# Kernel optimization log

Measured on AMD Instinct MI355X. Metric: run time of the kernel, lower is better.

## Reference

```python
import jax, jax.numpy as jnp
import numpy as np

B, L, SIZE, HEADS, AH, NBR, KER, DEPTH = 64, 512, 128, 8, 16, 15, 16, 3
MAXD = 20.0
N = B * L
EDGE = KER + 3 + 9 + 1  # 29


def _normalize(v):
    return v / (jnp.linalg.norm(v, axis=-1, keepdims=True) + 1e-8)


def _frames(pos):
    # local orientation frame per residue from consecutive CA displacements
    u = _normalize(pos[1:] - pos[:-1])            # (N-1,3)
    up = jnp.concatenate([u[:1], u], axis=0)      # u_{i-1}
    un = jnp.concatenate([u, u[-1:]], axis=0)     # u_i
    b = _normalize(up - un)
    n = _normalize(jnp.cross(up, un))
    return jnp.stack([b, n, jnp.cross(b, n)], axis=-1)  # (N,3,3)


def setup_inputs() -> dict:
    key = jax.random.key(0)
    ks = jax.random.split(key, 16)
    g = lambda i, shape, s=1.0: jax.random.normal(ks[i], shape, jnp.float32) * s
    return {
        "tertiary": g(0, (N, 3, 3), 10.0),
        "sequence": g(1, (N, 20)),
        "subgraph_indices": jnp.arange(N, dtype=jnp.int32) // L,
        "knn_noise": g(2, (B, L, L)),
        "embed_w": g(3, (27, SIZE), 0.1), "embed_b": jnp.zeros((SIZE,), jnp.float32),
        "wq": g(4, (DEPTH, SIZE, HEADS * AH), 0.08),
        "wk": g(5, (DEPTH, SIZE + EDGE, HEADS * AH), 0.08),
        "wv": g(6, (DEPTH, SIZE + EDGE, HEADS * AH), 0.08),
        "wo": g(7, (DEPTH, HEADS * AH, SIZE), 0.08),
        "mlp_w1": g(8, (DEPTH, SIZE, SIZE), 0.08), "mlp_b1": jnp.zeros((DEPTH, SIZE), jnp.float32),
        "mlp_w2": g(9, (DEPTH, SIZE, SIZE), 0.08), "mlp_b2": jnp.zeros((DEPTH, SIZE), jnp.float32),
        "mlp_w3": g(10, (DEPTH, SIZE, SIZE), 0.08), "mlp_b3": jnp.zeros((DEPTH, SIZE), jnp.float32),
        "pool_w": g(11, (4, SIZE, SIZE, 3), 0.05), "pool_b": jnp.zeros((4, SIZE), jnp.float32),
        "energy_w": g(12, (SIZE, 1), 0.1), "energy_b": jnp.zeros((1,), jnp.float32),
    }


def _forward(tertiary, sequence, knn_noise, embed_w, embed_b, wq, wk, wv, wo,
             mlp_w1, mlp_b1, mlp_w2, mlp_b2, mlp_w3, mlp_b3,
             pool_w, pool_b, energy_w, energy_b):
    pos = tertiary[:, 1]                                   # (N,3) CA positions
    R = _frames(pos)                                       # (N,3,3)
    # ---- kNN per contiguous protein group with noisy distances ----
    pg = pos.reshape(B, L, 3)
    dist = jnp.linalg.norm(pg[:, :, None] - pg[:, None, :], axis=-1)  # (B,L,L)
    closeness = -dist + 3.0 * knn_noise
    idx = jax.lax.top_k(closeness, NBR)[1]                 # (B,L,NBR) local
    nbr = (idx + (jnp.arange(B) * L)[:, None, None]).reshape(N, NBR)
    # ---- RBF relative encoding (RelativeStructure.message) ----
    dvec = pos[nbr] - pos[:, None]                         # (N,NBR,3)
    d = jnp.linalg.norm(dvec, axis=-1)                     # (N,NBR)
    mu = jnp.linspace(0.0, MAXD, KER)
    sigma = MAXD / KER
    rbf = jnp.exp(-(((d[..., None] - mu) / sigma) ** 2))   # (N,NBR,KER)
    dirs = jnp.einsum('nrc,nkr->nkc', R, dvec / (d[..., None] + 1e-8))
    relrot = jnp.einsum('nrc,nkrd->nkcd', R, R[nbr]).reshape(N, NBR, 9)
    ind = jnp.arange(N, dtype=tertiary.dtype)
    relind = (ind[nbr] - ind[:, None])[..., None]
    edge = jnp.concatenate([rbf, dirs, relrot, relind], axis=-1)  # (N,NBR,EDGE)
    # ---- structured graph-attention encoder ----
    h = jnp.ones((N, 27), tertiary.dtype) @ embed_w + embed_b
    inv_sqrt = 1.0 / np.sqrt(AH).astype(np.float32)
    for l in range(DEPTH):
        q = (h @ wq[l]).reshape(N, HEADS, AH)
        kv = jnp.concatenate([h[nbr], edge], axis=-1)      # (N,NBR,SIZE+EDGE)
        k = (kv @ wk[l]).reshape(N, NBR, HEADS, AH)
        v = (kv @ wv[l]).reshape(N, NBR, HEADS, AH)
        logits = jnp.einsum('nhd,nkhd->nhk', q, k) * inv_sqrt
        a = jax.nn.softmax(logits, axis=-1)
        o = jnp.einsum('nhk,nkhd->nhd', a, v).reshape(N, HEADS * AH) @ wo[l]
        h = h + o
        m = jax.nn.relu(h @ mlp_w1[l] + mlp_b1[l])
        m = jax.nn.relu(m @ mlp_w2[l] + mlp_b2[l])
        h = h + m @ mlp_w3[l] + mlp_b3[l]
    # ---- scatter-pad pool: residual conv + maxpool(2), x4, then length-sum ----
    x = h.reshape(B, L, SIZE).transpose(0, 2, 1)           # (B,SIZE,L)
    for i in range(4):
        y = jax.lax.conv_general_dilated(
            x, pool_w[i], (1,), ((1, 1),),
            dimension_numbers=('NCH', 'OIH', 'NCH')) + pool_b[i][None, :, None]
        x = x + jax.nn.leaky_relu(y, 0.01)
        Lc = x.shape[-1]
        x = x.reshape(B, SIZE, Lc // 2, 2).max(axis=-1)
    pooled = x.sum(axis=-1)                                # (B,SIZE)
    return pooled @ energy_w + energy_b                    # (B,1)


def reference(tertiary, sequence, subgraph_indices, knn_noise, embed_w, embed_b,
              wq, wk, wv, wo, mlp_w1, mlp_b1, mlp_w2, mlp_b2, mlp_w3, mlp_b3,
              pool_w, pool_b, energy_w, energy_b):
    # subgraph_indices encodes contiguous equal-size groups (arange // L)
    return _forward(tertiary, sequence, knn_noise, embed_w, embed_b, wq, wk, wv, wo,
                    mlp_w1, mlp_b1, mlp_w2, mlp_b2, mlp_w3, mlp_b3,
                    pool_w, pool_b, energy_w, energy_b)
```

## Files before the change

### kernel.cpp

```cpp
#include <hip/hip_runtime.h>
#include <math.h>

#define N_TOT 32768
#define NNBR 15
#define APW 8
#define ELP 36
#define ETP 20
#define PLP 20

#define KNB 4096
#define FRB 128
#define PRB 3392

typedef __attribute__((ext_vector_type(8))) _Float16 f16x8;
typedef __attribute__((ext_vector_type(2))) _Float16 f16x2;
typedef __attribute__((ext_vector_type(4))) float f32x4;

#define CBAR() __asm__ volatile("" ::: "memory")

__device__ __forceinline__ _Float16 f2h(float x) { return (_Float16)x; }

template <int CTRL>
__device__ __forceinline__ unsigned long long dpp_max_u64(unsigned long long x) {
  unsigned lo = (unsigned)__builtin_amdgcn_update_dpp(
      0, (int)(unsigned)x, CTRL, 0xf, 0xf, true);
  unsigned hi = (unsigned)__builtin_amdgcn_update_dpp(
      0, (int)(unsigned)(x >> 32), CTRL, 0xf, 0xf, true);
  unsigned long long y = ((unsigned long long)hi << 32) | lo;
  return y > x ? y : x;
}

__device__ __forceinline__ void ins3(unsigned long long k,
                                     unsigned long long& m1,
                                     unsigned long long& m2,
                                     unsigned long long& m3) {
  unsigned long long t1 = k > m1 ? k : m1;
  unsigned long long r1 = k > m1 ? m1 : k;
  unsigned long long t2 = r1 > m2 ? r1 : m2;
  unsigned long long r2 = r1 > m2 ? m2 : r1;
  unsigned long long t3 = r2 > m3 ? r2 : m3;
  m1 = t1; m2 = t2; m3 = t3;
}

__global__ __launch_bounds__(256) void k_pre(
    const float* __restrict__ tert, const float* __restrict__ noise,
    int* __restrict__ nbr, float* __restrict__ pos, float* __restrict__ R,
    const float* __restrict__ wq, const float* __restrict__ wk,
    const float* __restrict__ wv, const float* __restrict__ wo,
    const float* __restrict__ w1, const float* __restrict__ w2,
    const float* __restrict__ w3, _Float16* __restrict__ wbt,
    _Float16* __restrict__ wqk, _Float16* __restrict__ wpe,
    const float* __restrict__ pw, _Float16* __restrict__ wct,
    const float* __restrict__ ew, const float* __restrict__ ebias,
    _Float16* __restrict__ h) {
  __shared__ float posL[512 * 3];
  __shared__ float hvS[128];
  int bb = blockIdx.x, tid = threadIdx.x;
  if (bb < KNB) {
    int b = bb >> 6;
    int n0 = b << 9;
    for (int i = tid; i < 1536; i += 256) {
      int r = i / 3, c = i - r * 3;
      posL[i] = tert[(size_t)(n0 + r) * 9 + 3 + c];
    }
    __syncthreads();
    int wave = tid >> 6, lane = tid & 63;
    int l = lane & 31;
    int rloc = (bb & 63) * 8 + wave * 2 + (lane >> 5);
    int row = n0 + rloc;
    const float* nrow = noise + (size_t)row * 512;
    float pix = posL[rloc * 3 + 0];
    float piy = posL[rloc * 3 + 1];
    float piz = posL[rloc * 3 + 2];
    unsigned long long m1 = 0ull, m2 = 0ull, m3 = 0ull;
#pragma unroll
    for (int jj = 0; jj < 16; jj++) {
      int j = l + jj * 32;
      float dx = posL[j * 3 + 0] - pix;
      float dy = posL[j * 3 + 1] - piy;
      float dz = posL[j * 3 + 2] - piz;
      float c = -sqrtf(dx * dx + dy * dy + dz * dz) + 3.f * nrow[j];
      unsigned u = __float_as_uint(c);
      unsigned s = u ^ (unsigned)(((int)u >> 31) | (int)0x80000000);
      unsigned long long k = ((unsigned long long)s << 9) | (unsigned)(511 - j);
      ins3(k, m1, m2, m3);
    }
    int jmine = 0;
#pragma unroll 1
    for (int it = 0; it < NNBR; it++) {
      unsigned long long r = m1;
      r = dpp_max_u64<0x111>(r);
      r = dpp_max_u64<0x112>(r);
      r = dpp_max_u64<0x114>(r);
      r = dpp_max_u64<0x118>(r);
      r = dpp_max_u64<0x142>(r);
      unsigned gloA = (unsigned)__builtin_amdgcn_readlane((int)(unsigned)r, 31);
      unsigned ghiA = (unsigned)__builtin_amdgcn_readlane((int)(unsigned)(r >> 32), 31);
      unsigned gloB = (unsigned)__builtin_amdgcn_readlane((int)(unsigned)r, 63);
      unsigned ghiB = (unsigned)__builtin_amdgcn_readlane((int)(unsigned)(r >> 32), 63);
      int jA = 511 - (int)(gloA & 511u);
      int jB = 511 - (int)(gloB & 511u);
      int j = (lane & 32) ? jB : jA;
      if (l == it) jmine = j;
      bool win = ((j & 31) == l);
      if (win) { m1 = m2; m2 = m3; m3 = 0ull; }
      if (__any((int)(win && m1 == 0ull))) {
        if (win && m1 == 0ull) {
          unsigned long long gthr = (lane & 32)
              ? (((unsigned long long)ghiB << 32) | gloB)
              : (((unsigned long long)ghiA << 32) | gloA);
          unsigned long long a1 = 0ull, a2 = 0ull, a3 = 0ull;
#pragma unroll 1
          for (int jj = 0; jj < 16; jj++) {
            int j2 = l + jj * 32;
            float dx = posL[j2 * 3 + 0] - pix;
            float dy = posL[j2 * 3 + 1] - piy;
            float dz = posL[j2 * 3 + 2] - piz;
            float c = -sqrtf(dx * dx + dy * dy + dz * dz) + 3.f * nrow[j2];
            unsigned u = __float_as_uint(c);
            unsigned s = u ^ (unsigned)(((int)u >> 31) | (int)0x80000000);
            unsigned long long k = ((unsigned long long)s << 9) | (unsigned)(511 - j2);
            if (k < gthr) ins3(k, a1, a2, a3);
          }
          m1 = a1; m2 = a2; m3 = a3;
        }
      }
    }
    if (l < NNBR) nbr[(size_t)row * NNBR + l] = n0 + jmine;
  } else if (bb < KNB + FRB) {
    int n = (bb - KNB) * 256 + tid;
    if (n >= N_TOT) return;
    float px = tert[n * 9 + 3], py = tert[n * 9 + 4], pz = tert[n * 9 + 5];
    pos[n * 3 + 0] = px; pos[n * 3 + 1] = py; pos[n * 3 + 2] = pz;
    int i0 = (n > 0) ? (n - 1) : 0;
    int i1 = (n < N_TOT - 1) ? n : (N_TOT - 2);
    float ax = tert[(i0 + 1) * 9 + 3] - tert[i0 * 9 + 3];
    float ay = tert[(i0 + 1) * 9 + 4] - tert[i0 * 9 + 4];
    float az = tert[(i0 + 1) * 9 + 5] - tert[i0 * 9 + 5];
    float il = 1.f / (sqrtf(ax * ax + ay * ay + az * az) + 1e-8f);
    float ux = ax * il, uy = ay * il, uz = az * il;
    float cx = tert[(i1 + 1) * 9 + 3] - tert[i1 * 9 + 3];
    float cy = tert[(i1 + 1) * 9 + 4] - tert[i1 * 9 + 4];
    float cz = tert[(i1 + 1) * 9 + 5] - tert[i1 * 9 + 5];
    il = 1.f / (sqrtf(cx * cx + cy * cy + cz * cz) + 1e-8f);
    float vx = cx * il, vy = cy * il, vz = cz * il;
    float bx = ux - vx, by = uy - vy, bz = uz - vz;
    il = 1.f / (sqrtf(bx * bx + by * by + bz * bz) + 1e-8f);
    bx *= il; by *= il; bz *= il;
    float nx = uy * vz - uz * vy;
    float ny = uz * vx - ux * vz;
    float nz = ux * vy - uy * vx;
    il = 1.f / (sqrtf(nx * nx + ny * ny + nz * nz) + 1e-8f);
    nx *= il; ny *= il; nz *= il;
    float ex = by * nz - bz * ny;
    float ey = bz * nx - bx * nz;
    float ez = bx * ny - by * nx;
    float* Rn = R + (size_t)n * 9;
    Rn[0] = bx; Rn[1] = nx; Rn[2] = ex;
    Rn[3] = by; Rn[4] = ny; Rn[5] = ey;
    Rn[6] = bz; Rn[7] = nz; Rn[8] = ez;
  } else {
    int pb2 = bb - (KNB + FRB);
    if (pb2 < 1344) {
      int idx = pb2 * 256 + tid;
      int lL = idx / (7 * 16384);
      int r = idx % (7 * 16384);
      int w = r / 16384;
      int e = r % 16384;
      int k = e >> 7, n = e & 127;
      float val;
      switch (w) {
        case 0: val = wq[(size_t)lL * 16384 + e]; break;
        case 1: val = wk[(size_t)lL * 157 * 128 + e]; break;
        case 2: val = wv[(size_t)lL * 157 * 128 + e]; break;
        case 3: val = wo[(size_t)lL * 16384 + e]; break;
        case 4: val = w1[(size_t)lL * 16384 + e]; break;
        case 5: val = w2[(size_t)lL * 16384 + e]; break;
        default: val = w3[(size_t)lL * 16384 + e]; break;
      }
      wbt[(size_t)(lL * 7 + w) * 16384 + n * 128 + k] = f2h(val);
    } else if (pb2 < 1728) {
      int idx = (pb2 - 1344) * 256 + tid;
      int lL = idx / 32768;
      int r = idx % 32768;
      int blk = r >> 14;
      int jp = (r >> 7) & 127;
      int c = r & 127;
      int j = blk * 128 + jp;
      int hh = j >> 5, e = j & 31;
      float val = 0.f;
      if (e < 29) {
        const float* wqp = wq + (size_t)lL * 16384 + (size_t)c * 128 + hh * 16;
        const float* wkp = wk + (size_t)lL * 157 * 128 + (size_t)(128 + e) * 128 + hh * 16;
        float s = 0.f;
#pragma unroll
        for (int d = 0; d < 16; d++) s = fmaf(wqp[d], wkp[d], s);
        val = 0.25f * s;
      }
      wqk[(size_t)idx] = f2h(val);
    } else if (pb2 < 2112) {
      int idx = (pb2 - 1728) * 256 + tid;
      int lL = idx / 32768;
      int r = idx % 32768;
      int blk = r >> 14;
      int cout = (r >> 7) & 127;
      int jp = r & 127;
      int j = blk * 128 + jp;
      float val = 0.f;
      if (j < 232) {
        int e = j >> 3, hh = j & 7;
        const float* wvp = wv + (size_t)lL * 157 * 128 + (size_t)(128 + e) * 128 + hh * 16;
        const float* wop = wo + (size_t)lL * 16384 + (size_t)(hh * 16) * 128 + cout;
#pragma unroll
        for (int d = 0; d < 16; d++) val = fmaf(wvp[d], wop[d * 128], val);
      }
      wpe[(size_t)idx] = f2h(val);
    } else if (pb2 < 2880) {
      int idx = (pb2 - 2112) * 256 + tid;
      int kt = idx % 3;
      int rest = idx / 3;
      int i = rest % 128; rest /= 128;
      int oo = rest % 128;
      int s = rest / 128;
      wct[(((size_t)s * 3 + kt) * 128 + oo) * 128 + i] = f2h(pw[idx]);
    } else {
      int vb = pb2 - 2880;
      if (tid < 128) {
        float s = ebias[tid];
#pragma unroll
        for (int i = 0; i < 27; i++) s += ew[i * 128 + tid];
        hvS[tid] = s;
      }
      __syncthreads();
      size_t total = (size_t)N_TOT * 128;
      for (size_t j = (size_t)vb * 256 + tid; j < total; j += (size_t)512 * 256)
        h[j] = f2h(hvS[j & 127]);
    }
  }
}

__global__ __launch_bounds__(256) void k_edge(const float* __restrict__ pos,
                                              const float* __restrict__ R,
                                              const int* __restrict__ nbr,
                                              _Float16* __restrict__ edge) {
  int idx = blockIdx.x * 256 + threadIdx.x;
  if (idx >= N_TOT * NNBR) return;
  int n = idx / NNBR;
  int m = nbr[idx];
  float dx = pos[m * 3 + 0] - pos[n * 3 + 0];
  float dy = pos[m * 3 + 1] - pos[n * 3 + 1];
  float dz = pos[m * 3 + 2] - pos[n * 3 + 2];
  float d = sqrtf(dx * dx + dy * dy + dz * dz);
  _Float16 eb[32];
#pragma unroll
  for (int j = 0; j < 16; j++) {
    float mu = (20.f / 15.f) * (float)j;
    float t = (d - mu) * 0.8f;
    eb[j] = f2h(__expf(-t * t));
  }
  float inv = 1.f / (d + 1e-8f);
  float ux = dx * inv, uy = dy * inv, uz = dz * inv;
  float Rn[9], Rm[9];
#pragma unroll
  for (int j = 0; j < 9; j++) { Rn[j] = R[(size_t)n * 9 + j]; Rm[j] = R[(size_t)m * 9 + j]; }
#pragma unroll
  for (int cc = 0; cc < 3; cc++)
    eb[16 + cc] = f2h(Rn[0 * 3 + cc] * ux + Rn[1 * 3 + cc] * uy + Rn[2 * 3 + cc] * uz);
#pragma unroll
  for (int cc = 0; cc < 3; cc++)
#pragma unroll
    for (int dd = 0; dd < 3; dd++)
      eb[19 + cc * 3 + dd] = f2h(Rn[0 * 3 + cc] * Rm[0 * 3 + dd] +
                                 Rn[1 * 3 + cc] * Rm[1 * 3 + dd] +
                                 Rn[2 * 3 + cc] * Rm[2 * 3 + dd]);
  eb[28] = f2h((float)(m - n));
  eb[29] = (_Float16)0.f; eb[30] = (_Float16)0.f; eb[31] = (_Float16)0.f;
  _Float16* e = edge + (size_t)idx * 32;
#pragma unroll
  for (int v = 0; v < 4; v++)
    *(uint4*)(e + v * 8) = *(const uint4*)(&eb[v * 8]);
}

__device__ __forceinline__ void stage_w(const _Float16* __restrict__ W, _Float16* Ws, int tid) {
  for (int j = tid; j < 2048; j += 256) {
    int row = j >> 4, seg = (j & 15) * 8;
    *(uint4*)&Ws[row * 136 + seg] = *(const uint4*)(W + (size_t)row * 128 + seg);
  }
}
__device__ __forceinline__ void stage_x(const _Float16* __restrict__ src, _Float16* X,
                                        int tid, int rowstride) {
  for (int j = tid; j < 1024; j += 256) {
    int row = j >> 4, seg = (j & 15) * 8;
    *(uint4*)&X[row * 136 + seg] = *(const uint4*)(src + (size_t)row * rowstride + seg);
  }
}
template <bool RESET>
__device__ __forceinline__ void gemm_tile_t(const _Float16* X, const _Float16* Ws,
                                            int wrow, int l16, int quad, f32x4 acc[8]) {
  if (RESET) {
#pragma unroll
    for (int t = 0; t < 8; t++) acc[t] = (f32x4){0.f, 0.f, 0.f, 0.f};
  }
#pragma unroll
  for (int kk = 0; kk < 4; kk++) {
    f16x8 a = *(const f16x8*)&X[(wrow + l16) * 136 + kk * 32 + quad * 8];
#pragma unroll
    for (int t = 0; t < 8; t++) {
      f16x8 b = *(const f16x8*)&Ws[(t * 16 + l16) * 136 + kk * 32 + quad * 8];
      acc[t] = __builtin_amdgcn_mfma_f32_16x16x32_f16(a, b, acc[t], 0, 0, 0);
    }
  }
}

__global__ __launch_bounds__(256) void k_qkv(const _Float16* __restrict__ A,
                                             const _Float16* __restrict__ Wqt,
                                             const _Float16* __restrict__ Wkt,
                                             const _Float16* __restrict__ Wvt,
                                             const _Float16* __restrict__ Wqk0,
                                             const _Float16* __restrict__ Wqk1,
                                             _Float16* __restrict__ q, _Float16* __restrict__ hk,
                                             _Float16* __restrict__ hv, _Float16* __restrict__ qkw) {
  __shared__ _Float16 X[64 * 136];
  __shared__ _Float16 Ws[128 * 136];
  int tid = threadIdx.x, r0 = blockIdx.x * 64;
  int lane = tid & 63, quad = lane >> 4, l16 = lane & 15, wrow = (tid >> 6) * 16;
  stage_x(A + (size_t)r0 * 128, X, tid, 128);
  const _Float16* wts[5] = {Wqt, Wkt, Wvt, Wqk0, Wqk1};
  f32x4 acc[8];
  for (int w = 0; w < 5; w++) {
    __syncthreads();
    stage_w(wts[w], Ws, tid);
    __syncthreads();
    gemm_tile_t<true>(X, Ws, wrow, l16, quad, acc);
#pragma unroll
    for (int t = 0; t < 8; t++) {
      int col = t * 16 + l16;
#pragma unroll
      for (int r = 0; r < 4; r++) {
        float v = acc[t][r];
        int rowg = r0 + wrow + quad * 4 + r;
        if (w < 3) {
          _Float16* C = (w == 0) ? q : (w == 1) ? hk : hv;
          C[(size_t)rowg * 128 + col] = f2h(v);
        } else {
          qkw[(size_t)rowg * 256 + (w - 3) * 128 + col] = f2h(v);
        }
      }
    }
  }
}

__global__ __launch_bounds__(256) void k_post(const _Float16* __restrict__ o,
                                              const _Float16* __restrict__ pe_g,
                                              _Float16* __restrict__ h,
                                              const _Float16* __restrict__ Wot,
                                              const _Float16* __restrict__ Wpe0,
                                              const _Float16* __restrict__ Wpe1,
                                              const _Float16* __restrict__ W1t, const float* __restrict__ B1,
                                              const _Float16* __restrict__ W2t, const float* __restrict__ B2,
                                              const _Float16* __restrict__ W3t, const float* __restrict__ B3,
                                              const _Float16* __restrict__ Wqt,
                                              const _Float16* __restrict__ Wkt,
                                              const _Float16* __restrict__ Wvt,
                                              const _Float16* __restrict__ Wqk0,
                                              const _Float16* __restrict__ Wqk1,
                                              _Float16* __restrict__ qo, _Float16* __restrict__ hko,
                                              _Float16* __restrict__ hvo, _Float16* __restrict__ qkwo,
                                              int do_qkv) {
  __shared__ _Float16 X[64 * 136];
  __shared__ _Float16 Ws[128 * 136];
  int tid = threadIdx.x, r0 = blockIdx.x * 64;
  int lane = tid & 63, quad = lane >> 4, l16 = lane & 15, wrow = (tid >> 6) * 16;
  f32x4 acc[8], hres[8];
  stage_x(o + (size_t)r0 * 128, X, tid, 128);
  stage_w(Wot, Ws, tid);
  __syncthreads();
  gemm_tile_t<true>(X, Ws, wrow, l16, quad, acc);
  const _Float16* wpes[2] = {Wpe0, Wpe1};
#pragma unroll 1
  for (int blk = 0; blk < 2; blk++) {
    __syncthreads();
    stage_x(pe_g + (size_t)r0 * 256 + blk * 128, X, tid, 256);
    stage_w(wpes[blk], Ws, tid);
    __syncthreads();
    gemm_tile_t<false>(X, Ws, wrow, l16, quad, acc);
  }
#pragma unroll
  for (int t = 0; t < 8; t++) {
    int col = t * 16 + l16;
#pragma unroll
    for (int r = 0; r < 4; r++)
      hres[t][r] = acc[t][r] + (float)h[(size_t)(r0 + wrow + quad * 4 + r) * 128 + col];
  }
  __syncthreads();
#pragma unroll
  for (int t = 0; t < 8; t++) {
    int col = t * 16 + l16;
#pragma unroll
    for (int r = 0; r < 4; r++)
      X[(wrow + quad * 4 + r) * 136 + col] = f2h(hres[t][r]);
  }
  stage_w(W1t, Ws, tid);
  __syncthreads();
  gemm_tile_t<true>(X, Ws, wrow, l16, quad, acc);
  __syncthreads();
#pragma unroll
  for (int t = 0; t < 8; t++) {
    int col = t * 16 + l16; float bv = B1[col];
#pragma unroll
    for (int r = 0; r < 4; r++)
      X[(wrow + quad * 4 + r) * 136 + col] = f2h(fmaxf(acc[t][r] + bv, 0.f));
  }
  stage_w(W2t, Ws, tid);
  __syncthreads();
  gemm_tile_t<true>(X, Ws, wrow, l16, quad, acc);
  __syncthreads();
#pragma unroll
  for (int t = 0; t < 8; t++) {
    int col = t * 16 + l16; float bv = B2[col];
#pragma unroll
    for (int r = 0; r < 4; r++)
      X[(wrow + quad * 4 + r) * 136 + col] = f2h(fmaxf(acc[t][r] + bv, 0.f));
  }
  stage_w(W3t, Ws, tid);
  __syncthreads();
  gemm_tile_t<true>(X, Ws, wrow, l16, quad, acc);
  __syncthreads();
#pragma unroll
  for (int t = 0; t < 8; t++) {
    int col = t * 16 + l16; float bv = B3[col];
#pragma unroll
    for (int r = 0; r < 4; r++) {
      float v = hres[t][r] + acc[t][r] + bv;
      h[(size_t)(r0 + wrow + quad * 4 + r) * 128 + col] = f2h(v);
      if (do_qkv) X[(wrow + quad * 4 + r) * 136 + col] = f2h(v);
    }
  }
  if (!do_qkv) return;
  const _Float16* wts[5] = {Wqt, Wkt, Wvt, Wqk0, Wqk1};
  for (int w = 0; w < 5; w++) {
    __syncthreads();
    stage_w(wts[w], Ws, tid);
    __syncthreads();
    gemm_tile_t<true>(X, Ws, wrow, l16, quad, acc);
#pragma unroll
    for (int t = 0; t < 8; t++) {
      int col = t * 16 + l16;
#pragma unroll
      for (int r = 0; r < 4; r++) {
        float v = acc[t][r];
        int rowg = r0 + wrow + quad * 4 + r;
        if (w < 3) {
          _Float16* C = (w == 0) ? qo : (w == 1) ? hko : hvo;
          C[(size_t)rowg * 128 + col] = f2h(v);
        } else {
          qkwo[(size_t)rowg * 256 + (w - 3) * 128 + col] = f2h(v);
        }
      }
    }
  }
}

__global__ __launch_bounds__(256) void k_attn(const _Float16* __restrict__ q,
                                              const _Float16* __restrict__ hk,
                                              const _Float16* __restrict__ hv,
                                              const int* __restrict__ nbr,
                                              const _Float16* __restrict__ edge,
                                              const _Float16* __restrict__ qkw,
                                              _Float16* __restrict__ o,
                                              _Float16* __restrict__ pe_g) {
  __shared__ float elL[4][15 * ELP];
  __shared__ float etL[4][32 * ETP];
  __shared__ float plL[4][8 * PLP];
  __shared__ int nbL[4][16];
  int tid = threadIdx.x, wave = tid >> 6, lane = tid & 63;
  float* el = elL[wave]; float* et = etL[wave]; float* pl = plL[wave];
  int* nbl = nbL[wave];
  int h8 = lane & 7, k2 = lane >> 3, c2 = lane * 2, h5 = lane >> 3;
  int kst = lane >> 2, gst = lane & 3;
  if (lane < 32) et[lane * ETP + 15] = 0.f;
  int n0 = (blockIdx.x * 4 + wave) * APW;
#pragma unroll 1
  for (int ni = 0; ni < APW; ni++) {
    int n = n0 + ni;
    if (lane < 60) {
      f16x8 ev = *(const f16x8*)(edge + ((size_t)n * 15 + kst) * 32 + gst * 8);
      float e0 = (float)ev[0], e1 = (float)ev[1], e2 = (float)ev[2], e3 = (float)ev[3];
      float e4 = (float)ev[4], e5 = (float)ev[5], e6 = (float)ev[6], e7 = (float)ev[7];
      *(f32x4*)&el[kst * ELP + gst * 8]     = (f32x4){e0, e1, e2, e3};
      *(f32x4*)&el[kst * ELP + gst * 8 + 4] = (f32x4){e4, e5, e6, e7};
      int ebs = gst * 8;
      et[(ebs + 0) * ETP + kst] = e0; et[(ebs + 1) * ETP + kst] = e1;
      et[(ebs + 2) * ETP + kst] = e2; et[(ebs + 3) * ETP + kst] = e3;
      et[(ebs + 4) * ETP + kst] = e4; et[(ebs + 5) * ETP + kst] = e5;
      et[(ebs + 6) * ETP + kst] = e6; et[(ebs + 7) * ETP + kst] = e7;
    }
    if (lane < 15) nbl[lane] = nbr[(size_t)n * NNBR + lane];
    const _Float16* qs = qkw + (size_t)n * 256 + h8 * 32;
    f16x8 w0 = *(const f16x8*)qs, w1 = *(const f16x8*)(qs + 8);
    f16x8 w2 = *(const f16x8*)(qs + 16), w3 = *(const f16x8*)(qs + 24);
    float qw[32];
#pragma unroll
    for (int d = 0; d < 8; d++) {
      qw[d] = (float)w0[d]; qw[8 + d] = (float)w1[d];
      qw[16 + d] = (float)w2[d]; qw[24 + d] = (float)w3[d];
    }
    const _Float16* qp = q + (size_t)n * 128 + h8 * 16;
    f16x8 qa = *(const f16x8*)qp, qb = *(const f16x8*)(qp + 8);
    float q16[16];
#pragma unroll
    for (int d = 0; d < 8; d++) { q16[d] = (float)qa[d]; q16[8 + d] = (float)qb[d]; }
    CBAR();
#pragma unroll
    for (int p = 0; p < 2; p++) {
      int k = k2 + p * 8;
      if (k < 15) {
        int m = nbl[k];
        const _Float16* hkp = hk + (size_t)m * 128 + h8 * 16;
        f16x8 ha = *(const f16x8*)hkp, hb = *(const f16x8*)(hkp + 8);
        float dot = 0.f;
#pragma unroll
        for (int d = 0; d < 8; d++) dot = fmaf(q16[d], (float)ha[d], dot);
#pragma unroll
        for (int d = 0; d < 8; d++) dot = fmaf(q16[8 + d], (float)hb[d], dot);
        float ep = 0.f;
#pragma unroll
        for (int c = 0; c < 8; c++) {
          f32x4 e4 = *(const f32x4*)&el[k * ELP + c * 4];
          ep = fmaf(e4[0], qw[c * 4 + 0], ep);
          ep = fmaf(e4[1], qw[c * 4 + 1], ep);
          ep = fmaf(e4[2], qw[c * 4 + 2], ep);
          ep = fmaf(e4[3], qw[c * 4 + 3], ep);
        }
        pl[h8 * PLP + k] = fmaf(0.25f, dot, ep);
      } else {
        pl[h8 * PLP + 15] = -1e30f;
      }
    }
    CBAR();
    if (lane < 8) {
      float v[16];
      *(f32x4*)&v[0]  = *(const f32x4*)&pl[lane * PLP + 0];
      *(f32x4*)&v[4]  = *(const f32x4*)&pl[lane * PLP + 4];
      *(f32x4*)&v[8]  = *(const f32x4*)&pl[lane * PLP + 8];
      *(f32x4*)&v[12] = *(const f32x4*)&pl[lane * PLP + 12];
      float mx = v[0];
#pragma unroll
      for (int i = 1; i < 15; i++) mx = fmaxf(mx, v[i]);
      float s = 0.f;
#pragma unroll
      for (int i = 0; i < 16; i++) { v[i] = __expf(v[i] - mx); s += v[i]; }
      float inv = 1.f / s;
#pragma unroll
      for (int i = 0; i < 16; i++) v[i] *= inv;
      *(f32x4*)&pl[lane * PLP + 0]  = *(const f32x4*)&v[0];
      *(f32x4*)&pl[lane * PLP + 4]  = *(const f32x4*)&v[4];
      *(f32x4*)&pl[lane * PLP + 8]  = *(const f32x4*)&v[8];
      *(f32x4*)&pl[lane * PLP + 12] = *(const f32x4*)&v[12];
    }
    CBAR();
    _Float16* peo = pe_g + (size_t)n * 256;
#pragma unroll
    for (int p = 0; p < 4; p++) {
      int j = p * 64 + lane;
      float s = 0.f;
      if (j < 232) {
        int e = j >> 3, hh = j & 7;
        f32x4 p0 = *(const f32x4*)&pl[hh * PLP + 0];
        f32x4 p1 = *(const f32x4*)&pl[hh * PLP + 4];
        f32x4 p2 = *(const f32x4*)&pl[hh * PLP + 8];
        f32x4 p3 = *(const f32x4*)&pl[hh * PLP + 12];
        f32x4 t0 = *(const f32x4*)&et[e * ETP + 0];
        f32x4 t1 = *(const f32x4*)&et[e * ETP + 4];
        f32x4 t2 = *(const f32x4*)&et[e * ETP + 8];
        f32x4 t3 = *(const f32x4*)&et[e * ETP + 12];
        s = p0[0]*t0[0] + p0[1]*t0[1] + p0[2]*t0[2] + p0[3]*t0[3]
          + p1[0]*t1[0] + p1[1]*t1[1] + p1[2]*t1[2] + p1[3]*t1[3]
          + p2[0]*t2[0] + p2[1]*t2[1] + p2[2]*t2[2] + p2[3]*t2[3]
          + p3[0]*t3[0] + p3[1]*t3[1] + p3[2]*t3[2] + p3[3]*t3[3];
      }
      peo[j] = f2h(s);
    }
    float pk[16];
    *(f32x4*)&pk[0]  = *(const f32x4*)&pl[h5 * PLP + 0];
    *(f32x4*)&pk[4]  = *(const f32x4*)&pl[h5 * PLP + 4];
    *(f32x4*)&pk[8]  = *(const f32x4*)&pl[h5 * PLP + 8];
    *(f32x4*)&pk[12] = *(const f32x4*)&pl[h5 * PLP + 12];
    float ox = 0.f, oy = 0.f;
#pragma unroll
    for (int k = 0; k < 15; k++) {
      int m = nbl[k];
      f16x2 hh = *(const f16x2*)(hv + (size_t)m * 128 + c2);
      ox = fmaf(pk[k], (float)hh[0], ox);
      oy = fmaf(pk[k], (float)hh[1], oy);
    }
    *(f16x2*)(o + (size_t)n * 128 + c2) = (f16x2){f2h(ox), f2h(oy)};
    CBAR();
  }
}

__global__ __launch_bounds__(256) void k_convpool_m(const _Float16* __restrict__ x,
                                                    const _Float16* __restrict__ Wc,
                                                    const float* __restrict__ bias,
                                                    _Float16* __restrict__ outp, int Tin) {
  __shared__ _Float16 Xs[66 * 136];
  __shared__ _Float16 Ws[128 * 136];
  int tid = threadIdx.x;
  int b = blockIdx.y;
  int t0 = blockIdx.x * 64;
  for (int j = tid; j < 66 * 16; j += 256) {
    int row = j >> 4, seg = (j & 15) * 8;
    int t = t0 - 1 + row;
    uint4 v = {0u, 0u, 0u, 0u};
    if (t >= 0 && t < Tin) v = *(const uint4*)(x + ((size_t)b * Tin + t) * 128 + seg);
    *(uint4*)&Xs[row * 136 + seg] = v;
  }
  int lane = tid & 63, quad = lane >> 4, l16 = lane & 15, wrow = (tid >> 6) * 16;
  f32x4 acc[8];
#pragma unroll
  for (int t = 0; t < 8; t++) acc[t] = (f32x4){0.f, 0.f, 0.f, 0.f};
  for (int kt = 0; kt < 3; kt++) {
    __syncthreads();
    stage_w(Wc + (size_t)kt * 16384, Ws, tid);
    __syncthreads();
#pragma unroll
    for (int kk = 0; kk < 4; kk++) {
      f16x8 a = *(const f16x8*)&Xs[(wrow + l16 + kt) * 136 + kk * 32 + quad * 8];
#pragma unroll
      for (int t = 0; t < 8; t++) {
        f16x8 bfr = *(const f16x8*)&Ws[(t * 16 + l16) * 136 + kk * 32 + quad * 8];
        acc[t] = __builtin_amdgcn_mfma_f32_16x16x32_f16(a, bfr, acc[t], 0, 0, 0);
      }
    }
  }
  int Tout = Tin >> 1;
#pragma unroll
  for (int t = 0; t < 8; t++) {
    int col = t * 16 + l16;
    float bv = bias[col];
#pragma unroll
    for (int rp = 0; rp < 2; rp++) {
      int rl0 = wrow + quad * 4 + rp * 2;
      float y0 = acc[t][rp * 2] + bv;
      float y1 = acc[t][rp * 2 + 1] + bv;
      float z0 = (float)Xs[(rl0 + 1) * 136 + col] + (y0 >= 0.f ? y0 : 0.01f * y0);
      float z1 = (float)Xs[(rl0 + 2) * 136 + col] + (y1 >= 0.f ? y1 : 0.01f * y1);
      outp[((size_t)b * Tout + ((t0 + rl0) >> 1)) * 128 + col] = f2h(fmaxf(z0, z1));
    }
  }
}

__global__ __launch_bounds__(128) void k_final(const _Float16* __restrict__ x,
                                               const float* __restrict__ ew,
                                               const float* __restrict__ ebb,
                                               float* __restrict__ outp) {
  int b = blockIdx.x, cc = threadIdx.x;
  float s = 0.f;
#pragma unroll
  for (int t = 0; t < 32; t++) s += (float)x[((size_t)b * 32 + t) * 128 + cc];
  float v = s * ew[cc];
#pragma unroll
  for (int m = 1; m < 64; m <<= 1) v += __shfl_xor(v, m);
  __shared__ float red[2];
  if ((cc & 63) == 0) red[cc >> 6] = v;
  __syncthreads();
  if (cc == 0) outp[b] = red[0] + red[1] + ebb[0];
}

extern "C" void kernel_launch(void* const* d_in, const int* in_sizes, int n_in,
                              void* d_out, int out_size, void* d_ws, size_t ws_size,
                              hipStream_t stream) {
  (void)in_sizes; (void)n_in; (void)out_size; (void)ws_size;
  const float* tert    = (const float*)d_in[0];
  const float* noise   = (const float*)d_in[3];
  const float* embed_w = (const float*)d_in[4];
  const float* embed_b = (const float*)d_in[5];
  const float* wq = (const float*)d_in[6];
  const float* wk = (const float*)d_in[7];
  const float* wv = (const float*)d_in[8];
  const float* wo = (const float*)d_in[9];
  const float* w1 = (const float*)d_in[10];
  const float* b1 = (const float*)d_in[11];
  const float* w2 = (const float*)d_in[12];
  const float* b2 = (const float*)d_in[13];
  const float* w3 = (const float*)d_in[14];
  const float* b3 = (const float*)d_in[15];
  const float* pw = (const float*)d_in[16];
  const float* pb = (const float*)d_in[17];
  const float* ew = (const float*)d_in[18];
  const float* eb = (const float*)d_in[19];
  float* outp = (float*)d_out;

  char* W = (char*)d_ws;
  float* pos  = (float*)W;        W += 393216;
  float* R    = (float*)W;        W += 1179648;
  int*   nbr  = (int*)W;          W += 1966080;
  _Float16* edge = (_Float16*)W;  W += 31457280;
  _Float16* h    = (_Float16*)W;  W += 8388608;
  _Float16* q    = (_Float16*)W;  W += 8388608;
  _Float16* hk   = (_Float16*)W;  W += 8388608;
  _Float16* hv   = (_Float16*)W;  W += 8388608;
  _Float16* o    = (_Float16*)W;  W += 8388608;
  _Float16* qkw_g = (_Float16*)W; W += 16777216;
  _Float16* pe_g  = (_Float16*)W; W += 16777216;
  _Float16* xa   = (_Float16*)W;  W += 4194304;
  _Float16* xb   = (_Float16*)W;  W += 2097152;
  _Float16* wbt  = (_Float16*)W;  W += 688128;
  _Float16* wqk  = (_Float16*)W;  W += 196608;
  _Float16* wpe  = (_Float16*)W;  W += 196608;
  _Float16* wct  = (_Float16*)W;  W += 393216;

  k_pre<<<KNB + FRB + PRB, 256, 0, stream>>>(tert, noise, nbr, pos, R,
                                             wq, wk, wv, wo, w1, w2, w3, wbt,
                                             wqk, wpe, pw, wct, embed_w, embed_b, h);
  k_edge<<<1920, 256, 0, stream>>>(pos, R, nbr, edge);

  const _Float16* wt[3][7];
  for (int l = 0; l < 3; l++)
    for (int w = 0; w < 7; w++) wt[l][w] = wbt + (size_t)(l * 7 + w) * 16384;
  const _Float16* wqk_l[3][2];
  const _Float16* wpe_l[3][2];
  for (int l = 0; l < 3; l++)
    for (int bk = 0; bk < 2; bk++) {
      wqk_l[l][bk] = wqk + (size_t)(l * 2 + bk) * 16384;
      wpe_l[l][bk] = wpe + (size_t)(l * 2 + bk) * 16384;
    }

  k_qkv<<<512, 256, 0, stream>>>(h, wt[0][0], wt[0][1], wt[0][2],
                                 wqk_l[0][0], wqk_l[0][1], q, hk, hv, qkw_g);
  for (int l = 0; l < 3; l++) {
    k_attn<<<1024, 256, 0, stream>>>(q, hk, hv, nbr, edge, qkw_g, o, pe_g);
    int nl = l + 1;
    int do_qkv = (nl < 3) ? 1 : 0;
    k_post<<<512, 256, 0, stream>>>(o, pe_g, h, wt[l][3],
                                    wpe_l[l][0], wpe_l[l][1],
                                    wt[l][4], b1 + l * 128,
                                    wt[l][5], b2 + l * 128,
                                    wt[l][6], b3 + l * 128,
                                    do_qkv ? wt[nl][0] : nullptr,
                                    do_qkv ? wt[nl][1] : nullptr,
                                    do_qkv ? wt[nl][2] : nullptr,
                                    do_qkv ? wqk_l[nl][0] : nullptr,
                                    do_qkv ? wqk_l[nl][1] : nullptr,
                                    q, hk, hv, qkw_g, do_qkv);
  }

  k_convpool_m<<<dim3(8, 64), 256, 0, stream>>>(h,  wct + 0 * 49152, pb + 0,   xa, 512);
  k_convpool_m<<<dim3(4, 64), 256, 0, stream>>>(xa, wct + 1 * 49152, pb + 128, xb, 256);
  k_convpool_m<<<dim3(2, 64), 256, 0, stream>>>(xb, wct + 2 * 49152, pb + 256, xa, 128);
  k_convpool_m<<<dim3(1, 64), 256, 0, stream>>>(xa, wct + 3 * 49152, pb + 384, xb, 64);
  k_final<<<64, 128, 0, stream>>>(xb, ew, eb, outp);
}
```

Baseline: 514.6 us.

## Use direct global-to-LDS weight loads with XOR swizzle and 32-bit kNN reduction

Weight tiles in the GEMM and conv-pool kernels are now staged with global_load_lds directly into an unpadded, XOR-swizzled LDS layout, replacing register-staged copies into a padded layout. This is meant to cut register traffic and instruction count for weight staging. The kNN top-k selection also changes from 64-bit packed keys to 32-bit values with separate indices, using a ballot and a 64-bit fallback only when values tie. That aims to halve the DPP reduction work per iteration, at the cost of extra tie-handling logic and correctness risk around the async LDS writes and barriers.

```diff
diff --git a/kernel.cpp b/kernel.cpp
--- a/kernel.cpp
+++ b/kernel.cpp
@@ -19,6 +19,12 @@
 #define CBAR() __asm__ volatile("" ::: "memory")
 
 __device__ __forceinline__ _Float16 f2h(float x) { return (_Float16)x; }
+
+template <int CTRL>
+__device__ __forceinline__ unsigned dpp_max_u32(unsigned x) {
+  unsigned y = (unsigned)__builtin_amdgcn_update_dpp(0, (int)x, CTRL, 0xf, 0xf, true);
+  return y > x ? y : x;
+}
 
 template <int CTRL>
 __device__ __forceinline__ unsigned long long dpp_max_u64(unsigned long long x) {
@@ -30,16 +36,18 @@
   return y > x ? y : x;
 }
 
-__device__ __forceinline__ void ins3(unsigned long long k,
-                                     unsigned long long& m1,
-                                     unsigned long long& m2,
-                                     unsigned long long& m3) {
-  unsigned long long t1 = k > m1 ? k : m1;
-  unsigned long long r1 = k > m1 ? m1 : k;
-  unsigned long long t2 = r1 > m2 ? r1 : m2;
-  unsigned long long r2 = r1 > m2 ? m2 : r1;
-  unsigned long long t3 = r2 > m3 ? r2 : m3;
-  m1 = t1; m2 = t2; m3 = t3;
+__device__ __forceinline__ void ins3v(unsigned s, int j,
+                                      unsigned& m1v, int& i1,
+                                      unsigned& m2v, int& i2,
+                                      unsigned& m3v, int& i3) {
+  bool g1 = s > m1v;
+  unsigned t = g1 ? m1v : s;  int it = g1 ? i1 : j;
+  m1v = g1 ? s : m1v;         i1  = g1 ? j  : i1;
+  bool g2 = t > m2v;
+  unsigned u = g2 ? m2v : t;  int iu = g2 ? i2 : it;
+  m2v = g2 ? t : m2v;         i2  = g2 ? it : i2;
+  bool g3 = u > m3v;
+  m3v = g3 ? u : m3v;         i3  = g3 ? iu : i3;
 }
 
 __global__ __launch_bounds__(256) void k_pre(
@@ -72,7 +80,8 @@
     float pix = posL[rloc * 3 + 0];
     float piy = posL[rloc * 3 + 1];
     float piz = posL[rloc * 3 + 2];
-    unsigned long long m1 = 0ull, m2 = 0ull, m3 = 0ull;
+    unsigned m1v = 0u, m2v = 0u, m3v = 0u;
+    int i1 = 0, i2 = 0, i3 = 0;
 #pragma unroll
     for (int jj = 0; jj < 16; jj++) {
       int j = l + jj * 32;
@@ -82,34 +91,46 @@
       float c = -sqrtf(dx * dx + dy * dy + dz * dz) + 3.f * nrow[j];
       unsigned u = __float_as_uint(c);
       unsigned s = u ^ (unsigned)(((int)u >> 31) | (int)0x80000000);
-      unsigned long long k = ((unsigned long long)s << 9) | (unsigned)(511 - j);
-      ins3(k, m1, m2, m3);
+      ins3v(s, j, m1v, i1, m2v, i2, m3v, i3);
     }
     int jmine = 0;
 #pragma unroll 1
     for (int it = 0; it < NNBR; it++) {
-      unsigned long long r = m1;
-      r = dpp_max_u64<0x111>(r);
-      r = dpp_max_u64<0x112>(r);
-      r = dpp_max_u64<0x114>(r);
-      r = dpp_max_u64<0x118>(r);
-      r = dpp_max_u64<0x142>(r);
-      unsigned gloA = (unsigned)__builtin_amdgcn_readlane((int)(unsigned)r, 31);
-      unsigned ghiA = (unsigned)__builtin_amdgcn_readlane((int)(unsigned)(r >> 32), 31);
-      unsigned gloB = (unsigned)__builtin_amdgcn_readlane((int)(unsigned)r, 63);
-      unsigned ghiB = (unsigned)__builtin_amdgcn_readlane((int)(unsigned)(r >> 32), 63);
-      int jA = 511 - (int)(gloA & 511u);
-      int jB = 511 - (int)(gloB & 511u);
+      unsigned r = m1v;
+      r = dpp_max_u32<0x111>(r);
+      r = dpp_max_u32<0x112>(r);
+      r = dpp_max_u32<0x114>(r);
+      r = dpp_max_u32<0x118>(r);
+      r = dpp_max_u32<0x142>(r);
+      unsigned gA = (unsigned)__builtin_amdgcn_readlane((int)r, 31);
+      unsigned gB = (unsigned)__builtin_amdgcn_readlane((int)r, 63);
+      unsigned gsel = (lane & 32) ? gB : gA;
+      bool match = (m1v == gsel);
+      unsigned long long mk = __ballot((int)match);
+      unsigned mA = (unsigned)mk, mB = (unsigned)(mk >> 32);
+      int jA = __builtin_amdgcn_readlane(i1, __ffs(mA) - 1);
+      int jB = __builtin_amdgcn_readlane(i1, 31 + __ffs(mB));
+      if (__popc(mA) > 1 || __popc(mB) > 1) {
+        unsigned long long pk = ((unsigned long long)m1v << 9) | (unsigned)(511 - i1);
+        pk = dpp_max_u64<0x111>(pk);
+        pk = dpp_max_u64<0x112>(pk);
+        pk = dpp_max_u64<0x114>(pk);
+        pk = dpp_max_u64<0x118>(pk);
+        pk = dpp_max_u64<0x142>(pk);
+        unsigned pA = (unsigned)__builtin_amdgcn_readlane((int)(unsigned)pk, 31);
+        unsigned pB = (unsigned)__builtin_amdgcn_readlane((int)(unsigned)pk, 63);
+        if (__popc(mA) > 1) jA = 511 - (int)(pA & 511u);
+        if (__popc(mB) > 1) jB = 511 - (int)(pB & 511u);
+      }
       int j = (lane & 32) ? jB : jA;
       if (l == it) jmine = j;
-      bool win = ((j & 31) == l);
-      if (win) { m1 = m2; m2 = m3; m3 = 0ull; }
-      if (__any((int)(win && m1 == 0ull))) {
-        if (win && m1 == 0ull) {
-          unsigned long long gthr = (lane & 32)
-              ? (((unsigned long long)ghiB << 32) | gloB)
-              : (((unsigned long long)ghiA << 32) | gloA);
-          unsigned long long a1 = 0ull, a2 = 0ull, a3 = 0ull;
+      bool win = match && (i1 == j);
+      if (win) { m1v = m2v; i1 = i2; m2v = m3v; i2 = i3; m3v = 0u; }
+      if (__any((int)(win && m1v == 0u))) {
+        if (win && m1v == 0u) {
+          unsigned gv = gsel; int gj = j;
+          unsigned a1 = 0u, a2 = 0u, a3 = 0u;
+          int b1i = 0, b2i = 0, b3i = 0;
 #pragma unroll 1
           for (int jj = 0; jj < 16; jj++) {
             int j2 = l + jj * 32;
@@ -119,10 +140,10 @@
             float c = -sqrtf(dx * dx + dy * dy + dz * dz) + 3.f * nrow[j2];
             unsigned u = __float_as_uint(c);
             unsigned s = u ^ (unsigned)(((int)u >> 31) | (int)0x80000000);
-            unsigned long long k = ((unsigned long long)s << 9) | (unsigned)(511 - j2);
-            if (k < gthr) ins3(k, a1, a2, a3);
+            bool keep = (s < gv) || (s == gv && j2 > gj);
+            ins3v(keep ? s : 0u, j2, a1, b1i, a2, b2i, a3, b3i);
           }
-          m1 = a1; m2 = a2; m3 = a3;
+          m1v = a1; i1 = b1i; m2v = a2; i2 = b2i; m3v = a3; i3 = b3i;
         }
       }
     }
@@ -281,10 +302,20 @@
     *(uint4*)(e + v * 8) = *(const uint4*)(&eb[v * 8]);
 }
 
-__device__ __forceinline__ void stage_w(const _Float16* __restrict__ W, _Float16* Ws, int tid) {
-  for (int j = tid; j < 2048; j += 256) {
-    int row = j >> 4, seg = (j & 15) * 8;
-    *(uint4*)&Ws[row * 136 + seg] = *(const uint4*)(W + (size_t)row * 128 + seg);
+__device__ __forceinline__ void stage_w_async(const _Float16* __restrict__ W,
+                                              _Float16* Ws, int tid) {
+  int wv = tid >> 6, lane = tid & 63;
+#pragma unroll
+  for (int it = 0; it < 8; it++) {
+    int base = it * 2048 + wv * 512;
+    int off = base + lane * 8;
+    int row = off >> 7;
+    int cL = (off >> 3) & 15;
+    int cS = cL ^ (row & 7);
+    const _Float16* src = W + ((size_t)row << 7) + (cS << 3);
+    __builtin_amdgcn_global_load_lds(
+        (const __attribute__((address_space(1))) void*)src,
+        (__attribute__((address_space(3))) void*)(Ws + base), 16, 0, 0);
   }
 }
 __device__ __forceinline__ void stage_x(const _Float16* __restrict__ src, _Float16* X,
@@ -306,7 +337,8 @@
     f16x8 a = *(const f16x8*)&X[(wrow + l16) * 136 + kk * 32 + quad * 8];
 #pragma unroll
     for (int t = 0; t < 8; t++) {
-      f16x8 b = *(const f16x8*)&Ws[(t * 16 + l16) * 136 + kk * 32 + quad * 8];
+      int rw = t * 16 + l16;
+      f16x8 b = *(const f16x8*)&Ws[(rw << 7) + ((((kk << 2) + quad) ^ (rw & 7)) << 3)];
       acc[t] = __builtin_amdgcn_mfma_f32_16x16x32_f16(a, b, acc[t], 0, 0, 0);
     }
   }
@@ -321,7 +353,7 @@
                                              _Float16* __restrict__ q, _Float16* __restrict__ hk,
                                              _Float16* __restrict__ hv, _Float16* __restrict__ qkw) {
   __shared__ _Float16 X[64 * 136];
-  __shared__ _Float16 Ws[128 * 136];
+  __shared__ _Float16 Ws[128 * 128];
   int tid = threadIdx.x, r0 = blockIdx.x * 64;
   int lane = tid & 63, quad = lane >> 4, l16 = lane & 15, wrow = (tid >> 6) * 16;
   stage_x(A + (size_t)r0 * 128, X, tid, 128);
@@ -329,7 +361,7 @@
   f32x4 acc[8];
   for (int w = 0; w < 5; w++) {
     __syncthreads();
-    stage_w(wts[w], Ws, tid);
+    stage_w_async(wts[w], Ws, tid);
     __syncthreads();
     gemm_tile_t<true>(X, Ws, wrow, l16, quad, acc);
 #pragma unroll
@@ -368,12 +400,12 @@
                                               _Float16* __restrict__ hvo, _Float16* __restrict__ qkwo,
                                               int do_qkv) {
   __shared__ _Float16 X[64 * 136];
-  __shared__ _Float16 Ws[128 * 136];
+  __shared__ _Float16 Ws[128 * 128];
   int tid = threadIdx.x, r0 = blockIdx.x * 64;
   int lane = tid & 63, quad = lane >> 4, l16 = lane & 15, wrow = (tid >> 6) * 16;
   f32x4 acc[8], hres[8];
   stage_x(o + (size_t)r0 * 128, X, tid, 128);
-  stage_w(Wot, Ws, tid);
+  stage_w_async(Wot, Ws, tid);
   __syncthreads();
   gemm_tile_t<true>(X, Ws, wrow, l16, quad, acc);
   const _Float16* wpes[2] = {Wpe0, Wpe1};
@@ -381,7 +413,7 @@
   for (int blk = 0; blk < 2; blk++) {
     __syncthreads();
     stage_x(pe_g + (size_t)r0 * 256 + blk * 128, X, tid, 256);
-    stage_w(wpes[blk], Ws, tid);
+    stage_w_async(wpes[blk], Ws, tid);
     __syncthreads();
     gemm_tile_t<false>(X, Ws, wrow, l16, quad, acc);
   }
@@ -400,7 +432,7 @@
     for (int r = 0; r < 4; r++)
       X[(wrow + quad * 4 + r) * 136 + col] = f2h(hres[t][r]);
   }
-  stage_w(W1t, Ws, tid);
+  stage_w_async(W1t, Ws, tid);
   __syncthreads();
   gemm_tile_t<true>(X, Ws, wrow, l16, quad, acc);
   __syncthreads();
@@ -411,7 +443,7 @@
     for (int r = 0; r < 4; r++)
       X[(wrow + quad * 4 + r) * 136 + col] = f2h(fmaxf(acc[t][r] + bv, 0.f));
   }
-  stage_w(W2t, Ws, tid);
+  stage_w_async(W2t, Ws, tid);
   __syncthreads();
   gemm_tile_t<true>(X, Ws, wrow, l16, quad, acc);
   __syncthreads();
@@ -422,7 +454,7 @@
     for (int r = 0; r < 4; r++)
       X[(wrow + quad * 4 + r) * 136 + col] = f2h(fmaxf(acc[t][r] + bv, 0.f));
   }
-  stage_w(W3t, Ws, tid);
+  stage_w_async(W3t, Ws, tid);
   __syncthreads();
   gemm_tile_t<true>(X, Ws, wrow, l16, quad, acc);
   __syncthreads();
@@ -440,7 +472,7 @@
   const _Float16* wts[5] = {Wqt, Wkt, Wvt, Wqk0, Wqk1};
   for (int w = 0; w < 5; w++) {
     __syncthreads();
-    stage_w(wts[w], Ws, tid);
+    stage_w_async(wts[w], Ws, tid);
     __syncthreads();
     gemm_tile_t<true>(X, Ws, wrow, l16, quad, acc);
 #pragma unroll
@@ -604,7 +636,7 @@
                                                     const float* __restrict__ bias,
                                                     _Float16* __restrict__ outp, int Tin) {
   __shared__ _Float16 Xs[66 * 136];
-  __shared__ _Float16 Ws[128 * 136];
+  __shared__ _Float16 Ws[128 * 128];
   int tid = threadIdx.x;
   int b = blockIdx.y;
   int t0 = blockIdx.x * 64;
@@ -621,14 +653,15 @@
   for (int t = 0; t < 8; t++) acc[t] = (f32x4){0.f, 0.f, 0.f, 0.f};
   for (int kt = 0; kt < 3; kt++) {
     __syncthreads();
-    stage_w(Wc + (size_t)kt * 16384, Ws, tid);
+    stage_w_async(Wc + (size_t)kt * 16384, Ws, tid);
     __syncthreads();
 #pragma unroll
     for (int kk = 0; kk < 4; kk++) {
       f16x8 a = *(const f16x8*)&Xs[(wrow + l16 + kt) * 136 + kk * 32 + quad * 8];
 #pragma unroll
       for (int t = 0; t < 8; t++) {
-        f16x8 bfr = *(const f16x8*)&Ws[(t * 16 + l16) * 136 + kk * 32 + quad * 8];
+        int rw = t * 16 + l16;
+        f16x8 bfr = *(const f16x8*)&Ws[(rw << 7) + ((((kk << 2) + quad) ^ (rw & 7)) << 3)];
         acc[t] = __builtin_amdgcn_mfma_f32_16x16x32_f16(a, bfr, acc[t], 0, 0, 0);
       }
     }
```

Result: faster. 455.5 us (-11.5%).
